# Performance work log

Measured on AMD Instinct MI355X. Metric: run time of the kernel, lower is better.

Reference implementation:

```python
import jax, jax.numpy as jnp
import numpy as np

B = 32768
D_IN = 512
D_OUT = 512
N_DIGITS = 9
N_LEVELS = N_DIGITS + 1


def _xavier_uniform(key, shape, gain):
    # nn.init.xavier_uniform_ on Linear weight of shape (out, in)
    fan_out, fan_in = shape
    limit = gain * np.sqrt(6.0 / (fan_in + fan_out))
    return jax.random.uniform(key, shape, jnp.float32, -limit, limit)


def setup_inputs() -> dict:
    key = jax.random.key(0)
    kx, kv, *kw = jax.random.split(key, 2 + N_LEVELS)
    x = jax.random.normal(kx, (B, D_IN), dtype=jnp.float32)
    valuations = jax.random.randint(kv, (B,), 0, N_LEVELS, dtype=jnp.int64)
    # level-aware xavier init: gain = 1/(1 + 0.1*level)
    W = jnp.stack([
        _xavier_uniform(kw[l], (D_OUT, D_IN), 1.0 / (1.0 + 0.1 * l))
        for l in range(N_LEVELS)
    ], axis=0)  # (L, out, in)
    level_gates = jnp.ones((N_LEVELS,), dtype=jnp.float32)
    cross_level_attn = (jnp.eye(N_LEVELS, dtype=jnp.float32) * 0.9
                        + jnp.ones((N_LEVELS, N_LEVELS), dtype=jnp.float32) * 0.01)
    bias = jnp.zeros((D_OUT,), dtype=jnp.float32)
    return {"x": x, "valuations": valuations, "W": W,
            "level_gates": level_gates, "cross_level_attn": cross_level_attn,
            "bias": bias}


def reference(x, valuations, W, level_gates, cross_level_attn, bias):
    val = jnp.clip(valuations, 0, N_DIGITS)  # (B,)
    # 10 per-level linears as one batched GEMM: (B, L, out)
    level_outputs = jnp.einsum('bi,loi->blo', x, W)
    gates = jax.nn.sigmoid(level_gates)  # (L,)
    level_outputs = level_outputs * gates[None, :, None]
    # per-sample gather of own valuation level -> (B, out)
    output = jnp.take_along_axis(level_outputs, val[:, None, None], axis=1)[:, 0, :]
    # soft cross-level attention combine
    attn_weights = jax.nn.softmax(cross_level_attn[val], axis=-1)  # (B, L)
    weighted = jnp.einsum('bl,blo->bo', attn_weights, level_outputs)
    output = 0.7 * output + 0.3 * weighted
    return output + bias
```

## Files before the change

kernel.cpp:

```cpp
#include <hip/hip_runtime.h>

#define B_N 32768
#define D 512
#define DD (D * D)
#define NLEV 10
#define TM 128
#define TN 256
#define BK 32
#define NHB 128
#define MROWS_MAX 34048
#define MAX_RT (MROWS_MAX / TM)

typedef unsigned short u16;
typedef short s16x8 __attribute__((ext_vector_type(8)));
typedef u16 u16x8 __attribute__((ext_vector_type(8)));
typedef float f32x4 __attribute__((ext_vector_type(4)));

__device__ __forceinline__ u16 f2bf(float f) {
  union { float f; unsigned u; } v; v.f = f;
  unsigned r = v.u + 0x7fffu + ((v.u >> 16) & 1u);
  return (u16)(r >> 16);
}
__device__ __forceinline__ int clampv(int v) {
  return v < 0 ? 0 : (v > NLEV - 1 ? NLEV - 1 : v);
}

__global__ void k1(const float* __restrict__ W, const float* __restrict__ lg,
                   const float* __restrict__ attn, const int* __restrict__ val,
                   u16* __restrict__ weff, u16* __restrict__ hist,
                   int* __restrict__ perm) {
  const int t = threadIdx.x;
  if (blockIdx.x < DD / 256) {
    __shared__ float c[NLEV * NLEV];
    if (t < NLEV) {
      float g[NLEV], a[NLEV], mx = -1e30f;
      #pragma unroll
      for (int l = 0; l < NLEV; ++l) {
        g[l] = 1.0f / (1.0f + expf(-lg[l]));
        a[l] = attn[t * NLEV + l];
        mx = fmaxf(mx, a[l]);
      }
      float s = 0.f;
      #pragma unroll
      for (int l = 0; l < NLEV; ++l) { a[l] = expf(a[l] - mx); s += a[l]; }
      float inv = 1.0f / s;
      #pragma unroll
      for (int l = 0; l < NLEV; ++l) {
        float cc = 0.3f * a[l] * inv * g[l];
        if (l == t) cc += 0.7f * g[t];
        c[t * NLEV + l] = cc;
      }
    }
    __syncthreads();
    const int idx = blockIdx.x * 256 + t;
    float w[NLEV];
    #pragma unroll
    for (int l = 0; l < NLEV; ++l) w[l] = W[l * DD + idx];
    #pragma unroll
    for (int v = 0; v < NLEV; ++v) {
      float s = 0.f;
      #pragma unroll
      for (int l = 0; l < NLEV; ++l) s += c[v * NLEV + l] * w[l];
      weff[v * DD + idx] = f2bf(s);
    }
  } else {
    __shared__ int lc[NLEV];
    const int b = blockIdx.x - DD / 256;
    if (t < NLEV) lc[t] = 0;
    __syncthreads();
    const int gid = b * 256 + t;
    atomicAdd(&lc[clampv(val[gid])], 1);
    perm[gid] = -1;
    if (b < (MROWS_MAX - B_N) / 256) perm[B_N + b * 256 + t] = -1;
    __syncthreads();
    if (t < NLEV) hist[b * NLEV + t] = (u16)lc[t];
  }
}

__global__ void k2(const int* __restrict__ val, const u16* __restrict__ hist,
                   int* __restrict__ perm, int* __restrict__ starts) {
  __shared__ int h[NHB * NLEV];
  __shared__ int st[NLEV + 1];
  __shared__ int cnt[NLEV];
  __shared__ int lc[NLEV];
  const int t = threadIdx.x, b = blockIdx.x;
  for (int i = t; i < NHB * NLEV; i += 256) h[i] = hist[i];
  if (t < NLEV) lc[t] = 0;
  __syncthreads();
  if (t < NLEV) {
    int run = 0;
    for (int bb = 0; bb < NHB; ++bb) {
      int x = h[bb * NLEV + t];
      h[bb * NLEV + t] = run;
      run += x;
    }
    cnt[t] = run;
  }
  __syncthreads();
  if (t == 0) {
    int s = 0;
    for (int v = 0; v < NLEV; ++v) {
      st[v] = s;
      s += (cnt[v] + TM - 1) & ~(TM - 1);
    }
    st[NLEV] = s;
  }
  __syncthreads();
  const int gid = b * 256 + t;
  const int v = clampv(val[gid]);
  const int pos = atomicAdd(&lc[v], 1);
  perm[st[v] + h[b * NLEV + v] + pos] = gid;
  if (b == 0 && t <= NLEV) starts[t] = st[t];
}

__global__ __launch_bounds__(512, 4) void k3(
    const float* __restrict__ x, const u16* __restrict__ weff,
    const int* __restrict__ perm, const int* __restrict__ starts,
    const float* __restrict__ bias, float* __restrict__ out) {
  __shared__ u16 As[TM * BK];
  __shared__ u16 Bs[TN * BK];

  const int ct = blockIdx.x, rt = blockIdx.y;
  const int Mpad = starts[NLEV];
  if (rt * TM >= Mpad) return;

  int v = 0;
  #pragma unroll
  for (int i = 1; i < NLEV; ++i) if (rt * TM >= starts[i]) v = i;

  const int tid = threadIdx.x;
  const int lane = tid & 63, wave = tid >> 6;
  const int wm = (wave >> 2) * 64, wn = (wave & 3) * 64;
  const int fm = lane & 15;
  const int cb = lane >> 4;

  const int ar = tid >> 2;
  const int ah = tid & 3;
  int prow = perm[rt * TM + ar];
  if (prow < 0) prow = 0;
  const float* xrow = x + (size_t)prow * D + ah * 8;
  const int sw = (ar >> 1) & 3;

  const u16* wb = weff + ((size_t)v * D + ct * TN) * D;

  f32x4 acc[4][4];
  #pragma unroll
  for (int i = 0; i < 4; ++i)
    #pragma unroll
    for (int j = 0; j < 4; ++j) acc[i][j] = (f32x4){0.f, 0.f, 0.f, 0.f};

  for (int k0 = 0; k0 < D; k0 += BK) {
    #pragma unroll
    for (int j = 0; j < 2; ++j) {
      const int c = j * 512 + wave * 64 + lane;
      const int n_ = c >> 2, slot = c & 3;
      const int kc = slot ^ ((n_ >> 1) & 3);
      const u16* g = wb + n_ * D + k0 + kc * 8;
      __builtin_amdgcn_global_load_lds(
          (const __attribute__((address_space(1))) void*)g,
          (__attribute__((address_space(3))) void*)(Bs + (j * 512 + wave * 64) * 8),
          16, 0, 0);
    }
    const f32x4* xp = (const f32x4*)(xrow + k0);
    f32x4 f0 = xp[0], f1 = xp[1];
    u16x8 c0;
    #pragma unroll
    for (int q = 0; q < 4; ++q) { c0[q] = f2bf(f0[q]); c0[4 + q] = f2bf(f1[q]); }
    *(u16x8*)(As + ar * BK + ((ah ^ sw) << 3)) = c0;
    __syncthreads();

    s16x8 af[4], bf[4];
    #pragma unroll
    for (int t4 = 0; t4 < 4; ++t4) {
      const int m = wm + t4 * 16 + fm;
      af[t4] = *(const s16x8*)(As + m * BK + ((cb ^ ((m >> 1) & 3)) << 3));
      const int n = wn + t4 * 16 + fm;
      bf[t4] = *(const s16x8*)(Bs + n * BK + ((cb ^ ((n >> 1) & 3)) << 3));
    }
    #pragma unroll
    for (int tm = 0; tm < 4; ++tm)
      #pragma unroll
      for (int tn = 0; tn < 4; ++tn)
        acc[tm][tn] = __builtin_amdgcn_mfma_f32_16x16x32_bf16(af[tm], bf[tn], acc[tm][tn], 0, 0, 0);
    __syncthreads();
  }

  float bv[4];
  #pragma unroll
  for (int tn = 0; tn < 4; ++tn) bv[tn] = bias[ct * TN + wn + tn * 16 + fm];
  #pragma unroll
  for (int tm = 0; tm < 4; ++tm) {
    #pragma unroll
    for (int r = 0; r < 4; ++r) {
      const int mrow = wm + tm * 16 + (lane >> 4) * 4 + r;
      const int p = perm[rt * TM + mrow];
      if (p >= 0) {
        float* o = out + (size_t)p * D + ct * TN + wn + fm;
        #pragma unroll
        for (int tn = 0; tn < 4; ++tn)
          o[tn * 16] = acc[tm][tn][r] + bv[tn];
      }
    }
  }
}

extern "C" void kernel_launch(void* const* d_in, const int* in_sizes, int n_in,
                              void* d_out, int out_size, void* d_ws, size_t ws_size,
                              hipStream_t stream) {
  const float* x    = (const float*)d_in[0];
  const int*   val  = (const int*)d_in[1];
  const float* W    = (const float*)d_in[2];
  const float* lg   = (const float*)d_in[3];
  const float* attn = (const float*)d_in[4];
  const float* bias = (const float*)d_in[5];
  float* out = (float*)d_out;

  char* ws = (char*)d_ws;
  int* starts = (int*)(ws + 0);
  u16* hist   = (u16*)(ws + 64);
  int* perm   = (int*)(ws + 2688);
  u16* weff   = (u16*)(ws + 139264);

  k1<<<DD / 256 + NHB, 256, 0, stream>>>(W, lg, attn, val, weff, hist, perm);
  k2<<<NHB, 256, 0, stream>>>(val, hist, perm, starts);
  k3<<<dim3(D / TN, MAX_RT), 512, 0, stream>>>(x, weff, perm, starts, bias, out);
}
```

Measured before the change: 179.2 us.

## Double-buffer LDS tiles and prefetch next K-slice in GEMM main loop

The GEMM kernel now ping-pongs between two LDS buffers for the A and B tiles. The next weight tile's async global-to-LDS load and a register prefetch of x two steps ahead are issued before the MFMA work on the current tile. This cuts the K loop from two barriers per iteration to one and aims to hide global load latency behind compute. In exchange it doubles LDS use (to about 48KB per block) and adds registers for the prefetched x values, which may lower occupancy under the 4-block launch bound.

```diff
diff --git a/kernel.cpp b/kernel.cpp
--- a/kernel.cpp
+++ b/kernel.cpp
@@ -7,6 +7,7 @@
 #define TM 128
 #define TN 256
 #define BK 32
+#define NITER (D / BK)
 #define NHB 128
 #define MROWS_MAX 34048
 #define MAX_RT (MROWS_MAX / TM)
@@ -117,8 +118,8 @@
     const float* __restrict__ x, const u16* __restrict__ weff,
     const int* __restrict__ perm, const int* __restrict__ starts,
     const float* __restrict__ bias, float* __restrict__ out) {
-  __shared__ u16 As[TM * BK];
-  __shared__ u16 Bs[TN * BK];
+  __shared__ u16 As[2][TM * BK];
+  __shared__ u16 Bs[2][TN * BK];
 
   const int ct = blockIdx.x, rt = blockIdx.y;
   const int Mpad = starts[NLEV];
@@ -140,8 +141,16 @@
   if (prow < 0) prow = 0;
   const float* xrow = x + (size_t)prow * D + ah * 8;
   const int sw = (ar >> 1) & 3;
+  const int aslot = ar * BK + ((ah ^ sw) << 3);
 
   const u16* wb = weff + ((size_t)v * D + ct * TN) * D;
+  const int c0i = wave * 64 + lane;
+  const int c1i = 512 + c0i;
+  const int n0 = c0i >> 2, s0 = c0i & 3, kc0 = s0 ^ ((n0 >> 1) & 3);
+  const int n1 = c1i >> 2, s1 = c1i & 3, kc1 = s1 ^ ((n1 >> 1) & 3);
+  const u16* gb0 = wb + n0 * D + kc0 * 8;
+  const u16* gb1 = wb + n1 * D + kc1 * 8;
+  const int bdst0 = c0i * 8, bdst1 = c1i * 8;
 
   f32x4 acc[4][4];
   #pragma unroll
@@ -149,40 +158,66 @@
     #pragma unroll
     for (int j = 0; j < 4; ++j) acc[i][j] = (f32x4){0.f, 0.f, 0.f, 0.f};
 
-  for (int k0 = 0; k0 < D; k0 += BK) {
-    #pragma unroll
-    for (int j = 0; j < 2; ++j) {
-      const int c = j * 512 + wave * 64 + lane;
-      const int n_ = c >> 2, slot = c & 3;
-      const int kc = slot ^ ((n_ >> 1) & 3);
-      const u16* g = wb + n_ * D + k0 + kc * 8;
+  {
+    __builtin_amdgcn_global_load_lds(
+        (const __attribute__((address_space(1))) void*)gb0,
+        (__attribute__((address_space(3))) void*)(Bs[0] + bdst0), 16, 0, 0);
+    __builtin_amdgcn_global_load_lds(
+        (const __attribute__((address_space(1))) void*)gb1,
+        (__attribute__((address_space(3))) void*)(Bs[0] + bdst1), 16, 0, 0);
+    const f32x4* xp = (const f32x4*)xrow;
+    f32x4 f0 = xp[0], f1 = xp[1];
+    u16x8 cc;
+    #pragma unroll
+    for (int q = 0; q < 4; ++q) { cc[q] = f2bf(f0[q]); cc[4 + q] = f2bf(f1[q]); }
+    *(u16x8*)(As[0] + aslot) = cc;
+  }
+  f32x4 cf0, cf1;
+  {
+    const f32x4* xp = (const f32x4*)(xrow + BK);
+    cf0 = xp[0]; cf1 = xp[1];
+  }
+  __syncthreads();
+
+  int p = 0;
+  for (int i = 0; i < NITER; ++i) {
+    const bool hn = (i + 1 < NITER);
+    if (hn) {
+      const int k1o = (i + 1) * BK;
       __builtin_amdgcn_global_load_lds(
-          (const __attribute__((address_space(1))) void*)g,
-          (__attribute__((address_space(3))) void*)(Bs + (j * 512 + wave * 64) * 8),
-          16, 0, 0);
-    }
-    const f32x4* xp = (const f32x4*)(xrow + k0);
-    f32x4 f0 = xp[0], f1 = xp[1];
-    u16x8 c0;
-    #pragma unroll
-    for (int q = 0; q < 4; ++q) { c0[q] = f2bf(f0[q]); c0[4 + q] = f2bf(f1[q]); }
-    *(u16x8*)(As + ar * BK + ((ah ^ sw) << 3)) = c0;
-    __syncthreads();
-
+          (const __attribute__((address_space(1))) void*)(gb0 + k1o),
+          (__attribute__((address_space(3))) void*)(Bs[p ^ 1] + bdst0), 16, 0, 0);
+      __builtin_amdgcn_global_load_lds(
+          (const __attribute__((address_space(1))) void*)(gb1 + k1o),
+          (__attribute__((address_space(3))) void*)(Bs[p ^ 1] + bdst1), 16, 0, 0);
+    }
+    f32x4 nf0, nf1;
+    if (i + 2 < NITER) {
+      const f32x4* xp = (const f32x4*)(xrow + (i + 2) * BK);
+      nf0 = xp[0]; nf1 = xp[1];
+    }
     s16x8 af[4], bf[4];
     #pragma unroll
     for (int t4 = 0; t4 < 4; ++t4) {
       const int m = wm + t4 * 16 + fm;
-      af[t4] = *(const s16x8*)(As + m * BK + ((cb ^ ((m >> 1) & 3)) << 3));
+      af[t4] = *(const s16x8*)(As[p] + m * BK + ((cb ^ ((m >> 1) & 3)) << 3));
       const int n = wn + t4 * 16 + fm;
-      bf[t4] = *(const s16x8*)(Bs + n * BK + ((cb ^ ((n >> 1) & 3)) << 3));
+      bf[t4] = *(const s16x8*)(Bs[p] + n * BK + ((cb ^ ((n >> 1) & 3)) << 3));
     }
     #pragma unroll
     for (int tm = 0; tm < 4; ++tm)
       #pragma unroll
       for (int tn = 0; tn < 4; ++tn)
         acc[tm][tn] = __builtin_amdgcn_mfma_f32_16x16x32_bf16(af[tm], bf[tn], acc[tm][tn], 0, 0, 0);
-    __syncthreads();
+    if (hn) {
+      u16x8 cc;
+      #pragma unroll
+      for (int q = 0; q < 4; ++q) { cc[q] = f2bf(cf0[q]); cc[4 + q] = f2bf(cf1[q]); }
+      *(u16x8*)(As[p ^ 1] + aslot) = cc;
+      cf0 = nf0; cf1 = nf1;
+    }
+    __syncthreads();
+    p ^= 1;
   }
 
   float bv[4];
@@ -193,9 +228,9 @@
     #pragma unroll
     for (int r = 0; r < 4; ++r) {
       const int mrow = wm + tm * 16 + (lane >> 4) * 4 + r;
-      const int p = perm[rt * TM + mrow];
-      if (p >= 0) {
-        float* o = out + (size_t)p * D + ct * TN + wn + fm;
+      const int p2 = perm[rt * TM + mrow];
+      if (p2 >= 0) {
+        float* o = out + (size_t)p2 * D + ct * TN + wn + fm;
         #pragma unroll
         for (int tn = 0; tn < 4; ++tn)
           o[tn * 16] = acc[tm][tn][r] + bv[tn];
```

Result: faster. 174.0 us (-2.9%).
